# Performance work log

Hardware: AMD Instinct MI355X
Metric: run time of the kernel (lower is better)

Reference implementation:

```python
import jax, jax.numpy as jnp
import numpy as np

N = 50000        # nodes
E_RAND = 800000  # random edges; self-loops appended (A_hat = A + I)
IN = 512         # in_size
OUT = 64         # out_size per head
H = 8            # num_heads
NEG_SLOPE = 0.01 # torch F.leaky_relu default


def setup_inputs() -> dict:
    key = jax.random.key(0)
    k0, k1, k2, k3, k4, k5 = jax.random.split(key, 6)
    X = jax.random.normal(k0, (N, IN), jnp.float32)
    W = jax.random.normal(k1, (OUT * H, IN), jnp.float32) * (1.0 / np.sqrt(IN))
    b = jnp.zeros((OUT * H,), jnp.float32)
    a_l = jax.random.normal(k2, (1, OUT, H), jnp.float32) * 0.1
    a_r = jax.random.normal(k3, (1, OUT, H), jnp.float32) * 0.1
    # edges: random graph plus self-loops so every row segment is non-empty
    row = jnp.concatenate([jax.random.randint(k4, (E_RAND,), 0, N, jnp.int32),
                           jnp.arange(N, dtype=jnp.int32)])
    col = jnp.concatenate([jax.random.randint(k5, (E_RAND,), 0, N, jnp.int32),
                           jnp.arange(N, dtype=jnp.int32)])
    return {"X": X, "W": W, "b": b, "a_l": a_l, "a_r": a_r, "row": row, "col": col}


def reference(X, W, b, a_l, a_r, row, col):
    # dropout p=0.0 -> identity (eval-mode equivalent)
    Z = (X @ W.T + b).reshape(N, OUT, H)              # [N, OUT, H]
    e_l = jnp.sum(Z * a_l, axis=1)                    # [N, H]
    e_r = jnp.sum(Z * a_r, axis=1)                    # [N, H]
    e = jax.nn.leaky_relu(e_l[row] + e_r[col], NEG_SLOPE)  # [E, H]
    # segment softmax over edges grouped by destination row
    m = jax.ops.segment_max(e, row, num_segments=N)   # [N, H]
    ex = jnp.exp(e - m[row])                          # [E, H]
    denom = jax.ops.segment_sum(ex, row, num_segments=N)  # [N, H]
    a = ex / denom[row]                               # [E, H]
    # bspmm: out[i,:,h] = sum_{e: row[e]=i} a[e,h] * Z[col[e],:,h]
    msg = a[:, None, :] * Z[col]                      # [E, OUT, H]
    out = jax.ops.segment_sum(msg, row, num_segments=N)   # [N, OUT, H]
    return out
```

## Files before the change

kernel.cpp:

```cpp
#include <hip/hip_runtime.h>
#include <hip/hip_fp16.h>

#define IN_F 512
#define OH   512
#define NH   8

typedef _Float16 half_t;
typedef __attribute__((ext_vector_type(8))) _Float16 f16x8;
typedef __attribute__((ext_vector_type(4))) float    f32x4;

__global__ __launch_bounds__(256) void k_prep(const float* __restrict__ W,
                                              half_t* __restrict__ Wh, int nWe,
                                              const int* __restrict__ row,
                                              int* __restrict__ deg, int E,
                                              int nbW) {
  int b = blockIdx.x;
  if (b < nbW) {
    int i = (b * 256 + threadIdx.x) * 8;
    if (i >= nWe) return;
    float4 a = *(const float4*)(W + i);
    float4 c = *(const float4*)(W + i + 4);
    f16x8 h;
    h[0] = (half_t)a.x; h[1] = (half_t)a.y; h[2] = (half_t)a.z; h[3] = (half_t)a.w;
    h[4] = (half_t)c.x; h[5] = (half_t)c.y; h[6] = (half_t)c.z; h[7] = (half_t)c.w;
    *(f16x8*)(Wh + i) = h;
  } else {
    int e = (b - nbW) * 256 + threadIdx.x;
    if (e < E) atomicAdd(&deg[row[e]], 1);
  }
}

__global__ __launch_bounds__(512) void k_gemm16_v6(const float* __restrict__ X,
                                                   const half_t* __restrict__ Wh,
                                                   const float* __restrict__ bias,
                                                   const float* __restrict__ al,
                                                   const float* __restrict__ ar,
                                                   half_t* __restrict__ Zh,
                                                   float* __restrict__ el,
                                                   float* __restrict__ er,
                                                   int N, int nwg) {
  __shared__ half_t Bsm[128][516];
  const int tid  = threadIdx.x;
  const int lane = tid & 63;
  const int wid  = tid >> 6;

  int orig = blockIdx.x;
  int xcd = orig & 7;
  int q = nwg >> 3, r = nwg & 7;
  int start = (xcd < r) ? xcd * (q + 1) : r * (q + 1) + (xcd - r) * q;
  int work = start + (orig >> 3);
  const int n0 = (work >> 2) * 256;
  const int j0 = (work & 3) * 128;

  const int rl = lane & 15;
  const int hi16 = lane >> 4;

#pragma unroll
  for (int c = 0; c < 16; c++) {
    int col = wid * 16 + c;
    f16x8 v = *(const f16x8*)(Wh + (size_t)(j0 + col) * IN_F + lane * 8);
    *(f16x8*)&Bsm[col][lane * 8] = v;
  }
  __syncthreads();

  const float* aSrc[2];
#pragma unroll
  for (int m = 0; m < 2; m++) {
    int rr = n0 + wid * 32 + m * 16 + rl;
    if (rr >= N) rr = N - 1;
    aSrc[m] = X + (size_t)rr * IN_F + hi16 * 8;
  }

  f32x4 acc[2][8] = {};
  f32x4 ap[2][2][2];

#pragma unroll
  for (int m = 0; m < 2; m++) {
    ap[0][m][0] = *(const f32x4*)(aSrc[m] + 0);
    ap[0][m][1] = *(const f32x4*)(aSrc[m] + 4);
    ap[1][m][0] = *(const f32x4*)(aSrc[m] + 32);
    ap[1][m][1] = *(const f32x4*)(aSrc[m] + 36);
  }

#pragma unroll
  for (int k = 0; k < 16; k++) {
    f16x8 af[2];
#pragma unroll
    for (int m = 0; m < 2; m++) {
      f32x4 lo = ap[k & 1][m][0];
      f32x4 hi = ap[k & 1][m][1];
      f16x8 a;
#pragma unroll
      for (int u = 0; u < 4; u++) { a[u] = (half_t)lo[u]; a[u + 4] = (half_t)hi[u]; }
      af[m] = a;
    }
    if (k + 2 < 16) {
#pragma unroll
      for (int m = 0; m < 2; m++) {
        ap[k & 1][m][0] = *(const f32x4*)(aSrc[m] + (k + 2) * 32);
        ap[k & 1][m][1] = *(const f32x4*)(aSrc[m] + (k + 2) * 32 + 4);
      }
    }
#pragma unroll
    for (int n = 0; n < 8; n++) {
      f16x8 bf = *(const f16x8*)&Bsm[n * 16 + rl][k * 32 + hi16 * 8];
      acc[0][n] = __builtin_amdgcn_mfma_f32_16x16x32_f16(af[0], bf, acc[0][n], 0, 0, 0);
      acc[1][n] = __builtin_amdgcn_mfma_f32_16x16x32_f16(af[1], bf, acc[1][n], 0, 0, 0);
    }
  }

  float bv[8], av[8], rv[8];
#pragma unroll
  for (int n = 0; n < 8; n++) {
    int j = j0 + n * 16 + rl;
    bv[n] = bias[j]; av[n] = al[j]; rv[n] = ar[j];
  }

  float partl[2][4], partr[2][4];
#pragma unroll
  for (int m = 0; m < 2; m++)
#pragma unroll
    for (int qq = 0; qq < 4; qq++) { partl[m][qq] = 0.f; partr[m][qq] = 0.f; }

#pragma unroll
  for (int n = 0; n < 8; n++) {
    int j = j0 + n * 16 + rl;
#pragma unroll
    for (int m = 0; m < 2; m++) {
      int rbase = n0 + wid * 32 + m * 16 + hi16 * 4;
#pragma unroll
      for (int qq = 0; qq < 4; qq++) {
        float v = acc[m][n][qq] + bv[n];
        int nrow = rbase + qq;
        if (nrow < N) Zh[(size_t)nrow * OH + j] = (half_t)v;
        partl[m][qq] = fmaf(v, av[n], partl[m][qq]);
        partr[m][qq] = fmaf(v, rv[n], partr[m][qq]);
      }
    }
  }
  const int h = rl & 7;
#pragma unroll
  for (int m = 0; m < 2; m++) {
#pragma unroll
    for (int qq = 0; qq < 4; qq++) {
      float pl = partl[m][qq], pr = partr[m][qq];
      pl += __shfl_xor(pl, 8);
      pr += __shfl_xor(pr, 8);
      if (rl < 8) {
        int nrow = n0 + wid * 32 + m * 16 + hi16 * 4 + qq;
        if (nrow < N) {
          atomicAdd(&el[(size_t)nrow * NH + h], pl);
          atomicAdd(&er[(size_t)nrow * NH + h], pr);
        }
      }
    }
  }
}

#define SCAN_B 1024
__global__ __launch_bounds__(SCAN_B) void k_scan1(const int* __restrict__ deg,
                                                  int* __restrict__ off,
                                                  int* __restrict__ sums, int N) {
  __shared__ int s[SCAN_B];
  int tid = threadIdx.x;
  int g = blockIdx.x * SCAN_B + tid;
  int v = (g < N) ? deg[g] : 0;
  s[tid] = v;
  __syncthreads();
  for (int o = 1; o < SCAN_B; o <<= 1) {
    int t = (tid >= o) ? s[tid - o] : 0;
    __syncthreads();
    s[tid] += t;
    __syncthreads();
  }
  if (g < N) off[g] = s[tid] - v;
  if (tid == SCAN_B - 1) sums[blockIdx.x] = s[tid];
}

__global__ __launch_bounds__(SCAN_B) void k_scan3(int* __restrict__ off,
                                                  int* __restrict__ cursor,
                                                  const int* __restrict__ sums,
                                                  int nb, int N, int E) {
  __shared__ int sboff;
  int tid = threadIdx.x;
  if (tid < 64) {
    int v = (tid < nb && tid < (int)blockIdx.x) ? sums[tid] : 0;
#pragma unroll
    for (int s = 1; s < 64; s <<= 1) v += __shfl_xor(v, s);
    if (tid == 0) sboff = v;
  }
  __syncthreads();
  int g = blockIdx.x * SCAN_B + tid;
  if (g < N) {
    int v = off[g] + sboff;
    off[g] = v;
    cursor[g] = v;
  }
  if (g == 0) off[N] = E;
}

__global__ void k_fill(const int* __restrict__ row, const int* __restrict__ col,
                       int* __restrict__ cursor, int* __restrict__ colS, int E) {
  int e = blockIdx.x * blockDim.x + threadIdx.x;
  if (e < E) {
    int r = row[e];
    int p = atomicAdd(&cursor[r], 1);
    colS[p] = col[e];
  }
}

__global__ __launch_bounds__(256) void k_attagg(const half_t* __restrict__ Zh,
                                                const float* __restrict__ el,
                                                const float* __restrict__ er,
                                                const int* __restrict__ off,
                                                const int* __restrict__ colS,
                                                float* __restrict__ out, int N) {
  __shared__ float wts[4][64][NH];
  __shared__ int   cls[4][64];
  int wid = threadIdx.x >> 6, lane = threadIdx.x & 63;
  int i = blockIdx.x * 4 + wid;
  if (i >= N) return;
  int s = off[i], t = off[i + 1];
  int deg = t - s;

  float eli[8];
  {
    const float4* e4 = (const float4*)(el + (size_t)i * NH);
    float4 a = e4[0], b = e4[1];
    eli[0] = a.x; eli[1] = a.y; eli[2] = a.z; eli[3] = a.w;
    eli[4] = b.x; eli[5] = b.y; eli[6] = b.z; eli[7] = b.w;
  }

  float m[8], ehs[8];
  int csave = 0;
#pragma unroll
  for (int h = 0; h < 8; h++) m[h] = -1e30f;
  for (int p = s + lane; p < t; p += 64) {
    int c = __builtin_nontemporal_load(&colS[p]);
    csave = c;
    const float4* e4 = (const float4*)(er + (size_t)c * NH);
    float4 ea = e4[0], eb = e4[1];
    float ev[8] = {ea.x, ea.y, ea.z, ea.w, eb.x, eb.y, eb.z, eb.w};
#pragma unroll
    for (int h = 0; h < 8; h++) {
      float eh = eli[h] + ev[h];
      eh = (eh > 0.f) ? eh : 0.01f * eh;
      ehs[h] = eh;
      m[h] = fmaxf(m[h], eh);
    }
  }
#pragma unroll
  for (int st = 1; st < 64; st <<= 1)
#pragma unroll
    for (int h = 0; h < 8; h++) m[h] = fmaxf(m[h], __shfl_xor(m[h], st));

  float acc[8], den[8];
#pragma unroll
  for (int h = 0; h < 8; h++) { acc[h] = 0.f; den[h] = 0.f; }

  for (int base = s; base < t; base += 64) {
    int p = base + lane;
    if (p < t) {
      int c;
      float eh[8];
      if (deg <= 64) {
        c = csave;
#pragma unroll
        for (int h = 0; h < 8; h++) eh[h] = ehs[h];
      } else {
        c = __builtin_nontemporal_load(&colS[p]);
        const float4* e4 = (const float4*)(er + (size_t)c * NH);
        float4 ea = e4[0], eb = e4[1];
        float ev[8] = {ea.x, ea.y, ea.z, ea.w, eb.x, eb.y, eb.z, eb.w};
#pragma unroll
        for (int h = 0; h < 8; h++) {
          float e2 = eli[h] + ev[h];
          eh[h] = (e2 > 0.f) ? e2 : 0.01f * e2;
        }
      }
      cls[wid][lane] = c;
#pragma unroll
      for (int h = 0; h < 8; h++) {
        float pr = __expf(eh[h] - m[h]);
        den[h] += pr;
        wts[wid][lane][h] = pr;
      }
    }
    int cnt = t - base; if (cnt > 64) cnt = 64;

    int e = 0;
    for (; e + 4 <= cnt; e += 4) {
      int c0 = cls[wid][e + 0], c1 = cls[wid][e + 1];
      int c2 = cls[wid][e + 2], c3 = cls[wid][e + 3];
      f16x8 z0 = *(const f16x8*)(Zh + (size_t)c0 * OH + lane * 8);
      f16x8 z1 = *(const f16x8*)(Zh + (size_t)c1 * OH + lane * 8);
      f16x8 z2 = *(const f16x8*)(Zh + (size_t)c2 * OH + lane * 8);
      f16x8 z3 = *(const f16x8*)(Zh + (size_t)c3 * OH + lane * 8);
      const float* w0 = &wts[wid][e + 0][0];
      const float* w1 = &wts[wid][e + 1][0];
      const float* w2 = &wts[wid][e + 2][0];
      const float* w3 = &wts[wid][e + 3][0];
#pragma unroll
      for (int h = 0; h < 8; h++) {
        acc[h] = fmaf(w0[h], (float)z0[h], acc[h]);
        acc[h] = fmaf(w1[h], (float)z1[h], acc[h]);
        acc[h] = fmaf(w2[h], (float)z2[h], acc[h]);
        acc[h] = fmaf(w3[h], (float)z3[h], acc[h]);
      }
    }
    for (; e < cnt; e++) {
      int c = cls[wid][e];
      f16x8 z = *(const f16x8*)(Zh + (size_t)c * OH + lane * 8);
      const float* w = &wts[wid][e][0];
#pragma unroll
      for (int h = 0; h < 8; h++) acc[h] = fmaf(w[h], (float)z[h], acc[h]);
    }
  }

#pragma unroll
  for (int st = 1; st < 64; st <<= 1)
#pragma unroll
    for (int h = 0; h < 8; h++) den[h] += __shfl_xor(den[h], st);

  f32x4 o0, o1;
  o0[0] = acc[0] / den[0]; o0[1] = acc[1] / den[1];
  o0[2] = acc[2] / den[2]; o0[3] = acc[3] / den[3];
  o1[0] = acc[4] / den[4]; o1[1] = acc[5] / den[5];
  o1[2] = acc[6] / den[6]; o1[3] = acc[7] / den[7];
  __builtin_nontemporal_store(o0, (f32x4*)(out + (size_t)i * OH + lane * 8));
  __builtin_nontemporal_store(o1, (f32x4*)(out + (size_t)i * OH + lane * 8 + 4));
}

extern "C" void kernel_launch(void* const* d_in, const int* in_sizes, int n_in,
                              void* d_out, int out_size, void* d_ws, size_t ws_size,
                              hipStream_t stream) {
  const float* X    = (const float*)d_in[0];
  const float* W    = (const float*)d_in[1];
  const float* bias = (const float*)d_in[2];
  const float* a_l  = (const float*)d_in[3];
  const float* a_r  = (const float*)d_in[4];
  const int*   row  = (const int*)d_in[5];
  const int*   col  = (const int*)d_in[6];
  float* out = (float*)d_out;

  const int N = in_sizes[0] / IN_F;
  const int E = in_sizes[5];
  const int nWe = OH * IN_F;

  auto align_up = [](size_t v) { return (v + 255) & ~(size_t)255; };
  char* p = (char*)d_ws;
  half_t* Wh    = (half_t*)p; p += align_up((size_t)nWe * 2);
  half_t* Zh    = (half_t*)p; p += align_up((size_t)N * OH * 2);
  float* el     = (float*)p;  p += (size_t)N * NH * 4;
  float* er     = (float*)p;  p += align_up((size_t)N * NH * 4);
  int*   deg    = (int*)p;    p += align_up((size_t)N * 4);
  int*   off    = (int*)p;    p += align_up((size_t)(N + 1) * 4);
  int*   cursor = (int*)p;    p += align_up((size_t)N * 4);
  int*   sums   = (int*)p;    p += align_up((size_t)64 * 4);
  int*   colS   = (int*)p;    p += align_up((size_t)E * 4);
  (void)ws_size; (void)n_in; (void)out_size;

  const int nb = (N + SCAN_B - 1) / SCAN_B;

  hipMemsetAsync(deg, 0, (size_t)N * 4, stream);
  hipMemsetAsync(el, 0, (size_t)2 * N * NH * 4, stream);

  const int nbW = (nWe / 8 + 255) / 256;
  const int nbH = (E + 255) / 256;
  hipLaunchKernelGGL(k_prep, dim3(nbW + nbH), dim3(256), 0, stream,
                     W, Wh, nWe, row, deg, E, nbW);

  const int nwg = ((N + 255) / 256) * 4;
  hipLaunchKernelGGL(k_gemm16_v6, dim3(nwg), dim3(512), 0, stream,
                     X, Wh, bias, a_l, a_r, Zh, el, er, N, nwg);

  hipLaunchKernelGGL(k_scan1, dim3(nb), dim3(SCAN_B), 0, stream, deg, off, sums, N);
  hipLaunchKernelGGL(k_scan3, dim3(nb), dim3(SCAN_B), 0, stream,
                     off, cursor, sums, nb, N, E);
  hipLaunchKernelGGL(k_fill, dim3((E + 255) / 256), dim3(256), 0, stream,
                     row, col, cursor, colS, E);

  hipLaunchKernelGGL(k_attagg, dim3((N + 3) / 4), dim3(256), 0, stream,
                     Zh, el, er, off, colS, out, N);
}
```

Before: 332.0 us.

## Restructure GEMM to 128x512 tiles with double-buffered direct-to-LDS K-slices

The fused projection GEMM now has each workgroup compute 128 rows by all 512 output columns, instead of 256 rows by a 128-column slice with the whole K of W resident in LDS. The X and W tiles for each 32-wide K slice are streamed into double-buffered, XOR-swizzled LDS using global_load_lds, overlapping the next slice's loads with MFMAs on the current one. The aim is to read X from HBM once rather than four times and to cut LDS footprint so two workgroups can fit per CU. The cost is more accumulator registers per thread (4x8 tiles), two barriers per K step, and exact reliance on the vmcnt counts.

```diff
diff --git a/kernel.cpp b/kernel.cpp
--- a/kernel.cpp
+++ b/kernel.cpp
@@ -8,6 +8,13 @@
 typedef _Float16 half_t;
 typedef __attribute__((ext_vector_type(8))) _Float16 f16x8;
 typedef __attribute__((ext_vector_type(4))) float    f32x4;
+
+#define GLOBAL_AS const __attribute__((address_space(1))) void
+#define LDS_AS    __attribute__((address_space(3))) void
+
+__device__ static inline void gload_lds16(const void* g, void* l) {
+  __builtin_amdgcn_global_load_lds((GLOBAL_AS*)g, (LDS_AS*)l, 16, 0, 0);
+}
 
 __global__ __launch_bounds__(256) void k_prep(const float* __restrict__ W,
                                               half_t* __restrict__ Wh, int nWe,
@@ -30,104 +37,130 @@
   }
 }
 
-__global__ __launch_bounds__(512) void k_gemm16_v6(const float* __restrict__ X,
-                                                   const half_t* __restrict__ Wh,
-                                                   const float* __restrict__ bias,
-                                                   const float* __restrict__ al,
-                                                   const float* __restrict__ ar,
-                                                   half_t* __restrict__ Zh,
-                                                   float* __restrict__ el,
-                                                   float* __restrict__ er,
-                                                   int N, int nwg) {
-  __shared__ half_t Bsm[128][516];
+__global__ __launch_bounds__(512, 2) void k_gemm16_v7(const float* __restrict__ X,
+                                                      const half_t* __restrict__ Wh,
+                                                      const float* __restrict__ bias,
+                                                      const float* __restrict__ al,
+                                                      const float* __restrict__ ar,
+                                                      half_t* __restrict__ Zh,
+                                                      float* __restrict__ el,
+                                                      float* __restrict__ er,
+                                                      int N, int nwg) {
+  __shared__ float  As[2][128 * 32];
+  __shared__ half_t Bs[2][512 * 32];
   const int tid  = threadIdx.x;
   const int lane = tid & 63;
   const int wid  = tid >> 6;
+  const int wr = wid >> 2, wc = wid & 3;
 
   int orig = blockIdx.x;
   int xcd = orig & 7;
   int q = nwg >> 3, r = nwg & 7;
   int start = (xcd < r) ? xcd * (q + 1) : r * (q + 1) + (xcd - r) * q;
   int work = start + (orig >> 3);
-  const int n0 = (work >> 2) * 256;
-  const int j0 = (work & 3) * 128;
+  const int n0 = work * 128;
 
   const int rl = lane & 15;
   const int hi16 = lane >> 4;
 
-#pragma unroll
-  for (int c = 0; c < 16; c++) {
-    int col = wid * 16 + c;
-    f16x8 v = *(const f16x8*)(Wh + (size_t)(j0 + col) * IN_F + lane * 8);
-    *(f16x8*)&Bsm[col][lane * 8] = v;
-  }
-  __syncthreads();
-
-  const float* aSrc[2];
-#pragma unroll
-  for (int m = 0; m < 2; m++) {
-    int rr = n0 + wid * 32 + m * 16 + rl;
-    if (rr >= N) rr = N - 1;
-    aSrc[m] = X + (size_t)rr * IN_F + hi16 * 8;
-  }
-
-  f32x4 acc[2][8] = {};
-  f32x4 ap[2][2][2];
-
-#pragma unroll
-  for (int m = 0; m < 2; m++) {
-    ap[0][m][0] = *(const f32x4*)(aSrc[m] + 0);
-    ap[0][m][1] = *(const f32x4*)(aSrc[m] + 4);
-    ap[1][m][0] = *(const f32x4*)(aSrc[m] + 32);
-    ap[1][m][1] = *(const f32x4*)(aSrc[m] + 36);
-  }
-
-#pragma unroll
-  for (int k = 0; k < 16; k++) {
-    f16x8 af[2];
-#pragma unroll
-    for (int m = 0; m < 2; m++) {
-      f32x4 lo = ap[k & 1][m][0];
-      f32x4 hi = ap[k & 1][m][1];
+  int a_row[2], a_goff[2];
+#pragma unroll
+  for (int c = 0; c < 2; c++) {
+    int off = c * 8192 + wid * 1024 + lane * 16;
+    int rrow = off >> 7;
+    int sg = (off >> 4) & 7;
+    a_row[c]  = rrow;
+    a_goff[c] = (sg ^ (rrow & 7)) << 2;
+  }
+  int b_row[4], b_goff[4];
+#pragma unroll
+  for (int c = 0; c < 4; c++) {
+    int off = c * 8192 + wid * 1024 + lane * 16;
+    int jr = off >> 6;
+    int g  = (off >> 4) & 3;
+    b_row[c]  = jr;
+    b_goff[c] = (g ^ ((jr >> 1) & 3)) << 3;
+  }
+
+#define STAGE(BUF, KT)                                                          \
+  do {                                                                          \
+    _Pragma("unroll")                                                           \
+    for (int c = 0; c < 2; c++) {                                               \
+      int an = n0 + a_row[c]; if (an >= N) an = N - 1;                          \
+      const float* g = X + (size_t)an * IN_F + (KT) + a_goff[c];                \
+      gload_lds16(g, (char*)&As[BUF][0] + c * 8192 + wid * 1024);               \
+    }                                                                           \
+    _Pragma("unroll")                                                           \
+    for (int c = 0; c < 4; c++) {                                               \
+      const half_t* g = Wh + (size_t)b_row[c] * IN_F + (KT) + b_goff[c];        \
+      gload_lds16(g, (char*)&Bs[BUF][0] + c * 8192 + wid * 1024);               \
+    }                                                                           \
+  } while (0)
+
+  f32x4 acc[4][8] = {};
+
+  STAGE(0, 0);
+
+#pragma unroll
+  for (int ki = 0; ki < 16; ki++) {
+    const int cur = ki & 1;
+    if (ki < 15) {
+      STAGE(cur ^ 1, (ki + 1) * 32);
+      asm volatile("s_waitcnt vmcnt(6)" ::: "memory");
+    } else {
+      asm volatile("s_waitcnt vmcnt(0)" ::: "memory");
+    }
+    __builtin_amdgcn_sched_barrier(0);
+    __builtin_amdgcn_s_barrier();
+
+    f16x8 af[4], bf[8];
+#pragma unroll
+    for (int m = 0; m < 4; m++) {
+      int rr = wr * 64 + m * 16 + rl;
+      int r7 = rr & 7;
+      const char* base = (const char*)&As[cur][0] + rr * 128;
+      f32x4 lo = *(const f32x4*)(base + (((hi16 * 2) ^ r7) << 4));
+      f32x4 hi = *(const f32x4*)(base + (((hi16 * 2 + 1) ^ r7) << 4));
       f16x8 a;
 #pragma unroll
       for (int u = 0; u < 4; u++) { a[u] = (half_t)lo[u]; a[u + 4] = (half_t)hi[u]; }
       af[m] = a;
     }
-    if (k + 2 < 16) {
-#pragma unroll
-      for (int m = 0; m < 2; m++) {
-        ap[k & 1][m][0] = *(const f32x4*)(aSrc[m] + (k + 2) * 32);
-        ap[k & 1][m][1] = *(const f32x4*)(aSrc[m] + (k + 2) * 32 + 4);
-      }
-    }
 #pragma unroll
     for (int n = 0; n < 8; n++) {
-      f16x8 bf = *(const f16x8*)&Bsm[n * 16 + rl][k * 32 + hi16 * 8];
-      acc[0][n] = __builtin_amdgcn_mfma_f32_16x16x32_f16(af[0], bf, acc[0][n], 0, 0, 0);
-      acc[1][n] = __builtin_amdgcn_mfma_f32_16x16x32_f16(af[1], bf, acc[1][n], 0, 0, 0);
-    }
-  }
+      int jr = wc * 128 + n * 16 + rl;
+      bf[n] = *(const f16x8*)((const char*)&Bs[cur][0] + jr * 64 +
+                              ((hi16 ^ ((jr >> 1) & 3)) << 4));
+    }
+#pragma unroll
+    for (int m = 0; m < 4; m++)
+#pragma unroll
+      for (int n = 0; n < 8; n++)
+        acc[m][n] = __builtin_amdgcn_mfma_f32_16x16x32_f16(af[m], bf[n], acc[m][n], 0, 0, 0);
+
+    __builtin_amdgcn_s_barrier();
+  }
+#undef STAGE
 
   float bv[8], av[8], rv[8];
 #pragma unroll
   for (int n = 0; n < 8; n++) {
-    int j = j0 + n * 16 + rl;
+    int j = wc * 128 + n * 16 + rl;
     bv[n] = bias[j]; av[n] = al[j]; rv[n] = ar[j];
   }
 
-  float partl[2][4], partr[2][4];
-#pragma unroll
-  for (int m = 0; m < 2; m++)
+  float partl[4][4], partr[4][4];
+#pragma unroll
+  for (int m = 0; m < 4; m++)
 #pragma unroll
     for (int qq = 0; qq < 4; qq++) { partl[m][qq] = 0.f; partr[m][qq] = 0.f; }
 
 #pragma unroll
   for (int n = 0; n < 8; n++) {
-    int j = j0 + n * 16 + rl;
-#pragma unroll
-    for (int m = 0; m < 2; m++) {
-      int rbase = n0 + wid * 32 + m * 16 + hi16 * 4;
+    int j = wc * 128 + n * 16 + rl;
+#pragma unroll
+    for (int m = 0; m < 4; m++) {
+      int rbase = n0 + wr * 64 + m * 16 + hi16 * 4;
 #pragma unroll
       for (int qq = 0; qq < 4; qq++) {
         float v = acc[m][n][qq] + bv[n];
@@ -140,14 +173,14 @@
   }
   const int h = rl & 7;
 #pragma unroll
-  for (int m = 0; m < 2; m++) {
+  for (int m = 0; m < 4; m++) {
 #pragma unroll
     for (int qq = 0; qq < 4; qq++) {
       float pl = partl[m][qq], pr = partr[m][qq];
       pl += __shfl_xor(pl, 8);
       pr += __shfl_xor(pr, 8);
       if (rl < 8) {
-        int nrow = n0 + wid * 32 + m * 16 + hi16 * 4 + qq;
+        int nrow = n0 + wr * 64 + m * 16 + hi16 * 4 + qq;
         if (nrow < N) {
           atomicAdd(&el[(size_t)nrow * NH + h], pl);
           atomicAdd(&er[(size_t)nrow * NH + h], pr);
@@ -370,8 +403,8 @@
   hipLaunchKernelGGL(k_prep, dim3(nbW + nbH), dim3(256), 0, stream,
                      W, Wh, nWe, row, deg, E, nbW);
 
-  const int nwg = ((N + 255) / 256) * 4;
-  hipLaunchKernelGGL(k_gemm16_v6, dim3(nwg), dim3(512), 0, stream,
+  const int nwg = (N + 127) / 128;
+  hipLaunchKernelGGL(k_gemm16_v7, dim3(nwg), dim3(512), 0, stream,
                      X, Wh, bias, a_l, a_r, Zh, el, er, N, nwg);
 
   hipLaunchKernelGGL(k_scan1, dim3(nb), dim3(SCAN_B), 0, stream, deg, off, sums, N);
```

New measurement: 310.6 us. -6.4%, faster.
